# Optimization experiments

Hardware: AMD Instinct MI355X
Metric: run time of the kernel (lower is better)

Reference implementation:

```python
import jax, jax.numpy as jnp
import numpy as np

B, N, DIN = 32, 4096, 256
K, D, H = 8, 256, 512
ITERS = 3
EPS = 1e-8
LN_EPS = 1e-5
SCALE = D ** -0.5


def _ln(x, g, b):
    m = jnp.mean(x, axis=-1, keepdims=True)
    v = jnp.var(x, axis=-1, keepdims=True)
    return (x - m) * jax.lax.rsqrt(v + LN_EPS) * g + b


def setup_inputs() -> dict:
    key = jax.random.key(0)
    ks = jax.random.split(key, 12)
    lin = lambda k, o, i: jax.random.uniform(k, (o, i), jnp.float32, -1.0, 1.0) * (i ** -0.5)
    return {
        "x": jax.random.normal(ks[0], (B, N, DIN), jnp.float32),
        "noise": jax.random.normal(ks[1], (B, K, D), jnp.float32),
        "nx_g": jnp.ones((DIN,), jnp.float32), "nx_b": jnp.zeros((DIN,), jnp.float32),
        "ns_g": jnp.ones((D,), jnp.float32), "ns_b": jnp.zeros((D,), jnp.float32),
        "mu": jax.random.normal(ks[2], (1, 1, D), jnp.float32) * 0.02,
        "logsigma": jnp.zeros((1, 1, D), jnp.float32),
        "Wq": lin(ks[3], D, D), "Wk": lin(ks[4], D, DIN), "Wv": lin(ks[5], D, DIN),
        "W_ih": lin(ks[6], 3 * D, D), "W_hh": lin(ks[7], 3 * D, D),
        "b_ih": jnp.zeros((3 * D,), jnp.float32), "b_hh": jnp.zeros((3 * D,), jnp.float32),
        "mlp_g": jnp.ones((D,), jnp.float32), "mlp_b": jnp.zeros((D,), jnp.float32),
        "W1": lin(ks[8], H, D), "b1": jnp.zeros((H,), jnp.float32),
        "W2": lin(ks[9], D, H), "b2": jnp.zeros((D,), jnp.float32),
    }


def _gru(u, h, W_ih, W_hh, b_ih, b_hh):
    # PyTorch GRUCell: gates ordered (r, z, n)
    gi = u @ W_ih.T + b_ih   # [BK, 3D]
    gh = h @ W_hh.T + b_hh
    ir, iz, inn = jnp.split(gi, 3, axis=-1)
    hr, hz, hn = jnp.split(gh, 3, axis=-1)
    r = jax.nn.sigmoid(ir + hr)
    z = jax.nn.sigmoid(iz + hz)
    n = jnp.tanh(inn + r * hn)
    return (1.0 - z) * n + z * h


def reference(x, noise, nx_g, nx_b, ns_g, ns_b, mu, logsigma, Wq, Wk, Wv,
              W_ih, W_hh, b_ih, b_hh, mlp_g, mlp_b, W1, b1, W2, b2):
    xn = _ln(x, nx_g, nx_b)                       # [B,N,DIN]
    k = xn @ Wk.T                                 # [B,N,D]
    v = xn @ Wv.T                                 # [B,N,D]
    slots = mu + jnp.exp(logsigma) * noise        # [B,K,D]
    attn = None
    for _ in range(ITERS):
        s = _ln(slots, ns_g, ns_b)
        q = s @ Wq.T                              # [B,K,D]
        logits = jnp.einsum('bkd,bnd->bkn', q, k) * SCALE
        attn = jax.nn.softmax(logits, axis=1) + EPS   # softmax over slots
        attn = attn / jnp.sum(attn, axis=1, keepdims=True)
        updates = jnp.einsum('bkn,bnd->bkd', attn, v)
        h = _gru(updates.reshape(B * K, D), slots.reshape(B * K, D),
                 W_ih, W_hh, b_ih, b_hh).reshape(B, K, D)
        m = _ln(h, mlp_g, mlp_b)
        m = jax.nn.gelu(m @ W1.T + b1, approximate=False) @ W2.T + b2
        slots = h + m
    return slots, attn
```

## Files before the change

### kernel.cpp

```cpp
#include <hip/hip_runtime.h>
#include <hip/hip_bf16.h>
#include <math.h>

#define LN_EPS 1e-5f
#define EPSA 1e-8f
#define SCALE 0.0625f

typedef __attribute__((ext_vector_type(8))) short short8;
typedef __attribute__((ext_vector_type(4))) float f32x4;

__device__ inline void bf2x(unsigned int u, float& a, float& b) {
    union { unsigned int i; float f; } lo, hi;
    lo.i = u << 16; hi.i = u & 0xffff0000u;
    a = lo.f; b = hi.f;
}
__device__ inline float sigmoidf_(float x) { return 1.0f / (1.0f + expf(-x)); }
__device__ inline unsigned short f2bf(float f) {
    union { float f; unsigned int u; } v; v.f = f;
    unsigned int r = v.u + 0x7fffu + ((v.u >> 16) & 1u);
    return (unsigned short)(r >> 16);
}

__global__ __launch_bounds__(256) void row_stats(const float* __restrict__ x,
                                                 float* __restrict__ stats) {
    int w = threadIdx.x >> 6;
    int lane = threadIdx.x & 63;
    int r = blockIdx.x * 4 + w;
    const float4 xv = ((const float4*)(x + (size_t)r * 256))[lane];
    float s = xv.x + xv.y + xv.z + xv.w;
    float s2 = xv.x*xv.x + xv.y*xv.y + xv.z*xv.z + xv.w*xv.w;
    for (int off = 32; off > 0; off >>= 1) {
        s  += __shfl_down(s, off);
        s2 += __shfl_down(s2, off);
    }
    if (lane == 0) {
        float m = s * (1.0f/256.0f);
        float v = s2 * (1.0f/256.0f) - m * m;
        stats[2*r]   = m;
        stats[2*r+1] = rsqrtf(v + LN_EPS);
    }
}

__global__ __launch_bounds__(256) void pack_wb(const float* __restrict__ Wk,
                                               const float* __restrict__ Wv,
                                               __hip_bfloat16* __restrict__ Wcb) {
    int idx = blockIdx.x * 256 + threadIdx.x;
    int n = idx >> 8, k = idx & 255;
    float v = (n < 256) ? Wk[n*256 + k] : Wv[(n-256)*256 + k];
    Wcb[idx] = __float2bfloat16(v);
}

__global__ __launch_bounds__(256) void gemm_kv_mfma(const float* __restrict__ x,
                                                    const float* __restrict__ stats,
                                                    const float* __restrict__ nx_g,
                                                    const float* __restrict__ nx_b,
                                                    const __hip_bfloat16* __restrict__ Wcb,
                                                    __hip_bfloat16* __restrict__ kp,
                                                    __hip_bfloat16* __restrict__ vp) {
    __shared__ short As[128*64];
    __shared__ short Bs[128*64];
    const int t = threadIdx.x;
    const int row0 = blockIdx.x * 128;
    const int by = blockIdx.y;
    const int col0 = by * 128;
    const int l = t & 63, wid = t >> 6;
    const int wm = wid >> 1, wn = wid & 1;
    const int lr = l & 15, lk = (l >> 4) * 8;

    f32x4 acc[4][4];
    #pragma unroll
    for (int m = 0; m < 4; ++m)
        #pragma unroll
        for (int n = 0; n < 4; ++n) acc[m][n] = (f32x4){0.f, 0.f, 0.f, 0.f};

    for (int kt = 0; kt < 256; kt += 64) {
        #pragma unroll
        for (int j = 0; j < 4; ++j) {
            int g = j*256 + t;
            const __hip_bfloat16* src = Wcb + (size_t)(col0 + (g >> 3))*256 + kt + (g & 7)*8;
            __builtin_amdgcn_global_load_lds((const __attribute__((address_space(1))) void*)src,
                (__attribute__((address_space(3))) void*)(Bs + g*8), 16, 0, 0);
        }
        #pragma unroll
        for (int j = 0; j < 4; ++j) {
            int g = j*256 + t;
            int r = row0 + (g >> 3);
            int c = kt + (g & 7)*8;
            const float4* xs = (const float4*)(x + (size_t)r*256 + c);
            float4 v0 = xs[0], v1 = xs[1];
            float  mm = stats[2*r], rs = stats[2*r+1];
            const float4* gp = (const float4*)(nx_g + c);
            const float4* bp = (const float4*)(nx_b + c);
            float4 g0 = gp[0], g1 = gp[1], b0 = bp[0], b1 = bp[1];
            short8 o;
            o[0] = (short)f2bf((v0.x - mm)*rs*g0.x + b0.x);
            o[1] = (short)f2bf((v0.y - mm)*rs*g0.y + b0.y);
            o[2] = (short)f2bf((v0.z - mm)*rs*g0.z + b0.z);
            o[3] = (short)f2bf((v0.w - mm)*rs*g0.w + b0.w);
            o[4] = (short)f2bf((v1.x - mm)*rs*g1.x + b1.x);
            o[5] = (short)f2bf((v1.y - mm)*rs*g1.y + b1.y);
            o[6] = (short)f2bf((v1.z - mm)*rs*g1.z + b1.z);
            o[7] = (short)f2bf((v1.w - mm)*rs*g1.w + b1.w);
            *(short8*)&As[g*8] = o;
        }
        __syncthreads();

        #pragma unroll
        for (int kk = 0; kk < 64; kk += 32) {
            short8 af[4], bf[4];
            #pragma unroll
            for (int m = 0; m < 4; ++m)
                af[m] = *(const short8*)&As[(wm*64 + m*16 + lr)*64 + kk + lk];
            #pragma unroll
            for (int n = 0; n < 4; ++n)
                bf[n] = *(const short8*)&Bs[(wn*64 + n*16 + lr)*64 + kk + lk];
            #pragma unroll
            for (int m = 0; m < 4; ++m)
                #pragma unroll
                for (int n = 0; n < 4; ++n)
                    acc[m][n] = __builtin_amdgcn_mfma_f32_16x16x32_bf16(af[m], bf[n], acc[m][n], 0, 0, 0);
        }
        __syncthreads();
    }

    __hip_bfloat16* dst = (by < 2) ? kp : vp;
    const int colloc = col0 - ((by >= 2) ? 256 : 0);
    #pragma unroll
    for (int m = 0; m < 4; ++m)
        #pragma unroll
        for (int n = 0; n < 4; ++n) {
            #pragma unroll
            for (int jj = 0; jj < 4; ++jj) {
                int r = row0 + wm*64 + m*16 + (l >> 4)*4 + jj;
                int cc = colloc + wn*64 + n*16 + (l & 15);
                dst[(size_t)r*256 + cc] = __float2bfloat16(acc[m][n][jj]);
            }
        }
}

__global__ __launch_bounds__(256) void slots_init(const float* __restrict__ noise,
                                                  const float* __restrict__ mu,
                                                  const float* __restrict__ logsigma,
                                                  float* __restrict__ slots) {
    int i = blockIdx.x * 256 + threadIdx.x;
    int d = i & 255;
    slots[i] = mu[d] + expf(logsigma[d]) * noise[i];
}

__global__ __launch_bounds__(256) void qproj(const float* __restrict__ slots,
                                             const float* __restrict__ ns_g,
                                             const float* __restrict__ ns_b,
                                             const float* __restrict__ Wq,
                                             float* __restrict__ q) {
    int row = blockIdx.x, t = threadIdx.x;
    __shared__ float sn[256];
    __shared__ float red[8];
    float v = slots[row*256 + t];
    float s = v, s2 = v*v;
    for (int off = 32; off > 0; off >>= 1) {
        s  += __shfl_down(s, off);
        s2 += __shfl_down(s2, off);
    }
    if ((t & 63) == 0) { red[t>>6] = s; red[4 + (t>>6)] = s2; }
    __syncthreads();
    float S  = red[0]+red[1]+red[2]+red[3];
    float S2 = red[4]+red[5]+red[6]+red[7];
    float m = S * (1.0f/256.0f);
    float var = S2 * (1.0f/256.0f) - m*m;
    float rs = rsqrtf(var + LN_EPS);
    sn[t] = (v - m) * rs * ns_g[t] + ns_b[t];
    __syncthreads();
    float acc = 0.0f;
    const float4* wrow = (const float4*)(Wq + t*256);
    #pragma unroll 8
    for (int i = 0; i < 64; ++i) {
        float4 w = wrow[i];
        acc += w.x*sn[4*i] + w.y*sn[4*i+1] + w.z*sn[4*i+2] + w.w*sn[4*i+3];
    }
    q[row*256 + t] = acc;
}

__global__ __launch_bounds__(256) void attn_updates(const __hip_bfloat16* __restrict__ kp,
                                                    const __hip_bfloat16* __restrict__ vp,
                                                    const float* __restrict__ q,
                                                    float* __restrict__ attn_out,
                                                    float* __restrict__ partial) {
    int b = blockIdx.x >> 4, ch = blockIdx.x & 15, t = threadIdx.x;
    __shared__ float qs[8][256];
    __shared__ float as[8][256];
    #pragma unroll
    for (int j = 0; j < 8; ++j) qs[j][t] = q[(b*8 + j)*256 + t];
    __syncthreads();

    int n = ch*256 + t;
    const uint4* k4 = (const uint4*)(kp + ((size_t)b*4096 + n)*256);
    float lg[8] = {0,0,0,0,0,0,0,0};
    for (int i = 0; i < 32; ++i) {
        uint4 u = k4[i];
        float f[8];
        bf2x(u.x, f[0], f[1]); bf2x(u.y, f[2], f[3]);
        bf2x(u.z, f[4], f[5]); bf2x(u.w, f[6], f[7]);
        int d0 = i*8;
        #pragma unroll
        for (int kk = 0; kk < 8; ++kk) {
            float a = 0.0f;
            #pragma unroll
            for (int j = 0; j < 8; ++j) a += f[j] * qs[kk][d0 + j];
            lg[kk] += a;
        }
    }
    float mx = -1e30f;
    #pragma unroll
    for (int kk = 0; kk < 8; ++kk) { lg[kk] *= SCALE; mx = fmaxf(mx, lg[kk]); }
    float sum = 0.0f;
    #pragma unroll
    for (int kk = 0; kk < 8; ++kk) { lg[kk] = expf(lg[kk] - mx); sum += lg[kk]; }
    float inv = 1.0f / sum;
    const float renorm = 1.0f / (1.0f + 8.0f*EPSA);
    #pragma unroll
    for (int kk = 0; kk < 8; ++kk) {
        float a = (lg[kk]*inv + EPSA) * renorm;
        as[kk][t] = a;
        attn_out[((size_t)(b*8 + kk))*4096 + n] = a;
    }
    __syncthreads();

    int kk = t >> 5, dg = t & 31;
    float acc[8] = {0,0,0,0,0,0,0,0};
    const uint4* v4 = (const uint4*)(vp + ((size_t)b*4096 + ch*256)*256);
    #pragma unroll 4
    for (int nn = 0; nn < 256; ++nn) {
        float a = as[kk][nn];
        uint4 u = v4[nn*32 + dg];
        float f[8];
        bf2x(u.x, f[0], f[1]); bf2x(u.y, f[2], f[3]);
        bf2x(u.z, f[4], f[5]); bf2x(u.w, f[6], f[7]);
        #pragma unroll
        for (int j = 0; j < 8; ++j) acc[j] += a * f[j];
    }
    float* p = partial + (((size_t)(b*16 + ch)*8 + kk)*256) + dg*8;
    #pragma unroll
    for (int j = 0; j < 8; ++j) p[j] = acc[j];
}

__global__ __launch_bounds__(256) void gru(const float* __restrict__ partial,
                                           const float* __restrict__ slots,
                                           const float* __restrict__ W_ih,
                                           const float* __restrict__ W_hh,
                                           const float* __restrict__ b_ih,
                                           const float* __restrict__ b_hh,
                                           float* __restrict__ hprime) {
    int r = blockIdx.x, t = threadIdx.x;
    int b = r >> 3, k = r & 7;
    __shared__ float u_s[256], h_s[256];
    float u = 0.0f;
    #pragma unroll
    for (int ch = 0; ch < 16; ++ch)
        u += partial[(((size_t)(b*16 + ch)*8 + k)*256) + t];
    u_s[t] = u;
    h_s[t] = slots[r*256 + t];
    __syncthreads();

    float gi_r = b_ih[t], gi_z = b_ih[256 + t], gi_n = b_ih[512 + t];
    float gh_r = b_hh[t], gh_z = b_hh[256 + t], gh_n = b_hh[512 + t];
    const float4* wir = (const float4*)(W_ih + (size_t)t*256);
    const float4* wiz = (const float4*)(W_ih + (size_t)(256 + t)*256);
    const float4* win = (const float4*)(W_ih + (size_t)(512 + t)*256);
    const float4* whr = (const float4*)(W_hh + (size_t)t*256);
    const float4* whz = (const float4*)(W_hh + (size_t)(256 + t)*256);
    const float4* whn = (const float4*)(W_hh + (size_t)(512 + t)*256);
    #pragma unroll 4
    for (int i = 0; i < 64; ++i) {
        float u0 = u_s[4*i], u1 = u_s[4*i+1], u2 = u_s[4*i+2], u3 = u_s[4*i+3];
        float h0 = h_s[4*i], h1 = h_s[4*i+1], h2 = h_s[4*i+2], h3 = h_s[4*i+3];
        float4 w;
        w = wir[i]; gi_r += w.x*u0 + w.y*u1 + w.z*u2 + w.w*u3;
        w = wiz[i]; gi_z += w.x*u0 + w.y*u1 + w.z*u2 + w.w*u3;
        w = win[i]; gi_n += w.x*u0 + w.y*u1 + w.z*u2 + w.w*u3;
        w = whr[i]; gh_r += w.x*h0 + w.y*h1 + w.z*h2 + w.w*h3;
        w = whz[i]; gh_z += w.x*h0 + w.y*h1 + w.z*h2 + w.w*h3;
        w = whn[i]; gh_n += w.x*h0 + w.y*h1 + w.z*h2 + w.w*h3;
    }
    float rg = sigmoidf_(gi_r + gh_r);
    float zg = sigmoidf_(gi_z + gh_z);
    float ng = tanhf(gi_n + rg * gh_n);
    hprime[r*256 + t] = (1.0f - zg)*ng + zg*h_s[t];
}

__global__ __launch_bounds__(256) void mlp(const float* __restrict__ hprime,
                                           const float* __restrict__ mlp_g,
                                           const float* __restrict__ mlp_b,
                                           const float* __restrict__ W1,
                                           const float* __restrict__ b1,
                                           const float* __restrict__ W2,
                                           const float* __restrict__ b2,
                                           float* __restrict__ slots,
                                           float* __restrict__ out_slots,
                                           int last) {
    int r = blockIdx.x, t = threadIdx.x;
    __shared__ float hn[256];
    __shared__ float m1[512];
    __shared__ float red[8];
    float h = hprime[r*256 + t];
    float s = h, s2 = h*h;
    for (int off = 32; off > 0; off >>= 1) {
        s  += __shfl_down(s, off);
        s2 += __shfl_down(s2, off);
    }
    if ((t & 63) == 0) { red[t>>6] = s; red[4 + (t>>6)] = s2; }
    __syncthreads();
    float S  = red[0]+red[1]+red[2]+red[3];
    float S2 = red[4]+red[5]+red[6]+red[7];
    float m = S * (1.0f/256.0f);
    float var = S2 * (1.0f/256.0f) - m*m;
    float rs = rsqrtf(var + LN_EPS);
    hn[t] = (h - m) * rs * mlp_g[t] + mlp_b[t];
    __syncthreads();

    #pragma unroll
    for (int jj = 0; jj < 2; ++jj) {
        int j = t + jj*256;
        float acc = b1[j];
        const float4* w = (const float4*)(W1 + (size_t)j*256);
        #pragma unroll 8
        for (int i = 0; i < 64; ++i) {
            float4 wv = w[i];
            acc += wv.x*hn[4*i] + wv.y*hn[4*i+1] + wv.z*hn[4*i+2] + wv.w*hn[4*i+3];
        }
        m1[j] = 0.5f * acc * (1.0f + erff(acc * 0.70710678118654752f));
    }
    __syncthreads();

    float acc = b2[t];
    const float4* w2 = (const float4*)(W2 + (size_t)t*512);
    #pragma unroll 8
    for (int i = 0; i < 128; ++i) {
        float4 wv = w2[i];
        acc += wv.x*m1[4*i] + wv.y*m1[4*i+1] + wv.z*m1[4*i+2] + wv.w*m1[4*i+3];
    }
    float res = h + acc;
    slots[r*256 + t] = res;
    if (last) out_slots[r*256 + t] = res;
}

extern "C" void kernel_launch(void* const* d_in, const int* in_sizes, int n_in,
                              void* d_out, int out_size, void* d_ws, size_t ws_size,
                              hipStream_t stream) {
    const float* x        = (const float*)d_in[0];
    const float* noise    = (const float*)d_in[1];
    const float* nx_g     = (const float*)d_in[2];
    const float* nx_b     = (const float*)d_in[3];
    const float* ns_g     = (const float*)d_in[4];
    const float* ns_b     = (const float*)d_in[5];
    const float* mu       = (const float*)d_in[6];
    const float* logsigma = (const float*)d_in[7];
    const float* Wq       = (const float*)d_in[8];
    const float* Wk       = (const float*)d_in[9];
    const float* Wv       = (const float*)d_in[10];
    const float* W_ih     = (const float*)d_in[11];
    const float* W_hh     = (const float*)d_in[12];
    const float* b_ih     = (const float*)d_in[13];
    const float* b_hh     = (const float*)d_in[14];
    const float* mlp_g    = (const float*)d_in[15];
    const float* mlp_b    = (const float*)d_in[16];
    const float* W1       = (const float*)d_in[17];
    const float* b1       = (const float*)d_in[18];
    const float* W2       = (const float*)d_in[19];
    const float* b2       = (const float*)d_in[20];

    float* out_slots = (float*)d_out;
    float* out_attn  = (float*)d_out + 65536;

    char* ws = (char*)d_ws;
    float* stats = (float*)ws;
    __hip_bfloat16* Wcb = (__hip_bfloat16*)(stats + 262144);
    __hip_bfloat16* kp  = Wcb + 131072;
    __hip_bfloat16* vp  = kp + (size_t)33554432;
    float* slots  = (float*)(vp + (size_t)33554432);
    float* qbuf   = slots + 65536;
    float* partial= qbuf + 65536;
    float* hprime = partial + 1048576;

    row_stats<<<32768, 256, 0, stream>>>(x, stats);
    pack_wb<<<512, 256, 0, stream>>>(Wk, Wv, Wcb);
    dim3 g2(1024, 4);
    gemm_kv_mfma<<<g2, 256, 0, stream>>>(x, stats, nx_g, nx_b, Wcb, kp, vp);
    slots_init<<<256, 256, 0, stream>>>(noise, mu, logsigma, slots);

    for (int it = 0; it < 3; ++it) {
        qproj<<<256, 256, 0, stream>>>(slots, ns_g, ns_b, Wq, qbuf);
        attn_updates<<<512, 256, 0, stream>>>(kp, vp, qbuf, out_attn, partial);
        gru<<<256, 256, 0, stream>>>(partial, slots, W_ih, W_hh, b_ih, b_hh, hprime);
        mlp<<<256, 256, 0, stream>>>(hprime, mlp_g, mlp_b, W1, b1, W2, b2,
                                     slots, out_slots, it == 2);
    }
}
```

Measured before the change: 811.5 us.

## Fuse LayerNorm into KV GEMM, MFMA attention, and merge GRU with MLP

Removes the separate row-statistics pass by computing LayerNorm stats inside the K/V projection kernel, which now holds a full 64-row A tile in swizzled LDS and streams weights from global memory. Attention logits and the attention-weighted V sum move to bf16 MFMA, with q and attn split into high/low bf16 parts to preserve precision. The GRU and MLP kernels are merged to drop one launch and the hprime round trip. The risks are that V is loaded as a strided element gather and B operands bypass LDS.

Measured after the change: 836.1 us. +3.0%, slower.

```diff
diff --git a/kernel.cpp b/kernel.cpp
--- a/kernel.cpp
+++ b/kernel.cpp
@@ -7,39 +7,19 @@
 #define SCALE 0.0625f
 
 typedef __attribute__((ext_vector_type(8))) short short8;
+typedef __attribute__((ext_vector_type(4))) short short4_t;
 typedef __attribute__((ext_vector_type(4))) float f32x4;
 
-__device__ inline void bf2x(unsigned int u, float& a, float& b) {
-    union { unsigned int i; float f; } lo, hi;
-    lo.i = u << 16; hi.i = u & 0xffff0000u;
-    a = lo.f; b = hi.f;
-}
-__device__ inline float sigmoidf_(float x) { return 1.0f / (1.0f + expf(-x)); }
 __device__ inline unsigned short f2bf(float f) {
     union { float f; unsigned int u; } v; v.f = f;
     unsigned int r = v.u + 0x7fffu + ((v.u >> 16) & 1u);
     return (unsigned short)(r >> 16);
 }
-
-__global__ __launch_bounds__(256) void row_stats(const float* __restrict__ x,
-                                                 float* __restrict__ stats) {
-    int w = threadIdx.x >> 6;
-    int lane = threadIdx.x & 63;
-    int r = blockIdx.x * 4 + w;
-    const float4 xv = ((const float4*)(x + (size_t)r * 256))[lane];
-    float s = xv.x + xv.y + xv.z + xv.w;
-    float s2 = xv.x*xv.x + xv.y*xv.y + xv.z*xv.z + xv.w*xv.w;
-    for (int off = 32; off > 0; off >>= 1) {
-        s  += __shfl_down(s, off);
-        s2 += __shfl_down(s2, off);
-    }
-    if (lane == 0) {
-        float m = s * (1.0f/256.0f);
-        float v = s2 * (1.0f/256.0f) - m * m;
-        stats[2*r]   = m;
-        stats[2*r+1] = rsqrtf(v + LN_EPS);
-    }
-}
+__device__ inline float bf2f(unsigned short h) {
+    union { unsigned int u; float f; } v; v.u = ((unsigned int)h) << 16;
+    return v.f;
+}
+__device__ inline float sigmoidf_(float x) { return 1.0f / (1.0f + expf(-x)); }
 
 __global__ __launch_bounds__(256) void pack_wb(const float* __restrict__ Wk,
                                                const float* __restrict__ Wv,
@@ -50,92 +30,86 @@
     Wcb[idx] = __float2bfloat16(v);
 }
 
-__global__ __launch_bounds__(256) void gemm_kv_mfma(const float* __restrict__ x,
-                                                    const float* __restrict__ stats,
-                                                    const float* __restrict__ nx_g,
-                                                    const float* __restrict__ nx_b,
-                                                    const __hip_bfloat16* __restrict__ Wcb,
-                                                    __hip_bfloat16* __restrict__ kp,
-                                                    __hip_bfloat16* __restrict__ vp) {
-    __shared__ short As[128*64];
-    __shared__ short Bs[128*64];
+__global__ __launch_bounds__(256) void gemm_kv_fused(const float* __restrict__ x,
+                                                     const float* __restrict__ nx_g,
+                                                     const float* __restrict__ nx_b,
+                                                     const __hip_bfloat16* __restrict__ Wcb,
+                                                     __hip_bfloat16* __restrict__ kp,
+                                                     __hip_bfloat16* __restrict__ vp) {
+    __shared__ short As[64*256];
+    __shared__ float gb[512];
     const int t = threadIdx.x;
-    const int row0 = blockIdx.x * 128;
-    const int by = blockIdx.y;
-    const int col0 = by * 128;
-    const int l = t & 63, wid = t >> 6;
-    const int wm = wid >> 1, wn = wid & 1;
-    const int lr = l & 15, lk = (l >> 4) * 8;
-
-    f32x4 acc[4][4];
-    #pragma unroll
-    for (int m = 0; m < 4; ++m)
-        #pragma unroll
-        for (int n = 0; n < 4; ++n) acc[m][n] = (f32x4){0.f, 0.f, 0.f, 0.f};
-
-    for (int kt = 0; kt < 256; kt += 64) {
-        #pragma unroll
-        for (int j = 0; j < 4; ++j) {
-            int g = j*256 + t;
-            const __hip_bfloat16* src = Wcb + (size_t)(col0 + (g >> 3))*256 + kt + (g & 7)*8;
-            __builtin_amdgcn_global_load_lds((const __attribute__((address_space(1))) void*)src,
-                (__attribute__((address_space(3))) void*)(Bs + g*8), 16, 0, 0);
-        }
-        #pragma unroll
-        for (int j = 0; j < 4; ++j) {
-            int g = j*256 + t;
-            int r = row0 + (g >> 3);
-            int c = kt + (g & 7)*8;
-            const float4* xs = (const float4*)(x + (size_t)r*256 + c);
-            float4 v0 = xs[0], v1 = xs[1];
-            float  mm = stats[2*r], rs = stats[2*r+1];
-            const float4* gp = (const float4*)(nx_g + c);
-            const float4* bp = (const float4*)(nx_b + c);
-            float4 g0 = gp[0], g1 = gp[1], b0 = bp[0], b1 = bp[1];
-            short8 o;
-            o[0] = (short)f2bf((v0.x - mm)*rs*g0.x + b0.x);
-            o[1] = (short)f2bf((v0.y - mm)*rs*g0.y + b0.y);
-            o[2] = (short)f2bf((v0.z - mm)*rs*g0.z + b0.z);
-            o[3] = (short)f2bf((v0.w - mm)*rs*g0.w + b0.w);
-            o[4] = (short)f2bf((v1.x - mm)*rs*g1.x + b1.x);
-            o[5] = (short)f2bf((v1.y - mm)*rs*g1.y + b1.y);
-            o[6] = (short)f2bf((v1.z - mm)*rs*g1.z + b1.z);
-            o[7] = (short)f2bf((v1.w - mm)*rs*g1.w + b1.w);
-            *(short8*)&As[g*8] = o;
-        }
-        __syncthreads();
-
-        #pragma unroll
-        for (int kk = 0; kk < 64; kk += 32) {
-            short8 af[4], bf[4];
+    const int row0 = blockIdx.x * 64;
+    const int r = t >> 2, q = t & 3;
+
+    float4 xr[16];
+    const float* xrow = x + (size_t)(row0 + r) * 256 + q*4;
+    #pragma unroll
+    for (int j = 0; j < 16; ++j) xr[j] = *(const float4*)(xrow + j*16);
+    gb[t] = nx_g[t]; gb[t+256] = nx_b[t];
+
+    float s = 0.f, s2 = 0.f;
+    #pragma unroll
+    for (int j = 0; j < 16; ++j) {
+        s  += xr[j].x + xr[j].y + xr[j].z + xr[j].w;
+        s2 += xr[j].x*xr[j].x + xr[j].y*xr[j].y + xr[j].z*xr[j].z + xr[j].w*xr[j].w;
+    }
+    s  += __shfl_xor(s, 1);  s2 += __shfl_xor(s2, 1);
+    s  += __shfl_xor(s, 2);  s2 += __shfl_xor(s2, 2);
+    float m = s * (1.0f/256.0f);
+    float var = s2 * (1.0f/256.0f) - m*m;
+    float rstd = rsqrtf(var + LN_EPS);
+    __syncthreads();
+
+    #pragma unroll
+    for (int j = 0; j < 16; ++j) {
+        int c = q*4 + j*16;
+        float4 g = *(const float4*)&gb[c];
+        float4 bb = *(const float4*)&gb[256 + c];
+        short4_t o;
+        o[0] = (short)f2bf((xr[j].x - m)*rstd*g.x + bb.x);
+        o[1] = (short)f2bf((xr[j].y - m)*rstd*g.y + bb.y);
+        o[2] = (short)f2bf((xr[j].z - m)*rstd*g.z + bb.z);
+        o[3] = (short)f2bf((xr[j].w - m)*rstd*g.w + bb.w);
+        int byte = ((r << 9) + (c << 1)) ^ ((r & 7) << 4);
+        *(short4_t*)((char*)As + byte) = o;
+    }
+    __syncthreads();
+
+    const int l = t & 63, w = t >> 6;
+    const int lr = l & 15, lk = l >> 4;
+    const int arow = w*16 + lr;
+    short8 af[8];
+    #pragma unroll
+    for (int ks = 0; ks < 8; ++ks) {
+        int lin = (arow << 9) + (lk << 4) + (ks << 6);
+        af[ks] = *(short8*)((char*)As + (lin ^ ((arow & 7) << 4)));
+    }
+    for (int c = 0; c < 8; ++c) {
+        f32x4 acc[4];
+        #pragma unroll
+        for (int bf = 0; bf < 4; ++bf) acc[bf] = (f32x4){0.f,0.f,0.f,0.f};
+        #pragma unroll
+        for (int ks = 0; ks < 8; ++ks) {
             #pragma unroll
-            for (int m = 0; m < 4; ++m)
-                af[m] = *(const short8*)&As[(wm*64 + m*16 + lr)*64 + kk + lk];
-            #pragma unroll
-            for (int n = 0; n < 4; ++n)
-                bf[n] = *(const short8*)&Bs[(wn*64 + n*16 + lr)*64 + kk + lk];
-            #pragma unroll
-            for (int m = 0; m < 4; ++m)
-                #pragma unroll
-                for (int n = 0; n < 4; ++n)
-                    acc[m][n] = __builtin_amdgcn_mfma_f32_16x16x32_bf16(af[m], bf[n], acc[m][n], 0, 0, 0);
-        }
-        __syncthreads();
-    }
-
-    __hip_bfloat16* dst = (by < 2) ? kp : vp;
-    const int colloc = col0 - ((by >= 2) ? 256 : 0);
-    #pragma unroll
-    for (int m = 0; m < 4; ++m)
-        #pragma unroll
-        for (int n = 0; n < 4; ++n) {
+            for (int bf = 0; bf < 4; ++bf) {
+                const short8 bv = *(const short8*)((const short*)Wcb +
+                    ((size_t)(c*64 + bf*16 + lr))*256 + ks*32 + lk*8);
+                acc[bf] = __builtin_amdgcn_mfma_f32_16x16x32_bf16(af[ks], bv, acc[bf], 0, 0, 0);
+            }
+        }
+        __hip_bfloat16* dst = (c < 4) ? kp : vp;
+        const int cb = c*64 - ((c >= 4) ? 256 : 0);
+        #pragma unroll
+        for (int bf = 0; bf < 4; ++bf) {
+            int col = cb + bf*16 + lr;
             #pragma unroll
             for (int jj = 0; jj < 4; ++jj) {
-                int r = row0 + wm*64 + m*16 + (l >> 4)*4 + jj;
-                int cc = colloc + wn*64 + n*16 + (l & 15);
-                dst[(size_t)r*256 + cc] = __float2bfloat16(acc[m][n][jj]);
+                int row = row0 + w*16 + lk*4 + jj;
+                dst[(size_t)row*256 + col] = __float2bfloat16(acc[bf][jj]);
             }
         }
+    }
 }
 
 __global__ __launch_bounds__(256) void slots_init(const float* __restrict__ noise,
@@ -151,8 +125,9 @@
                                              const float* __restrict__ ns_g,
                                              const float* __restrict__ ns_b,
                                              const float* __restrict__ Wq,
-                                             float* __restrict__ q) {
+                                             unsigned short* __restrict__ qb) {
     int row = blockIdx.x, t = threadIdx.x;
+    int b = row >> 3, s8 = row & 7;
     __shared__ float sn[256];
     __shared__ float red[8];
     float v = slots[row*256 + t];
@@ -177,88 +152,147 @@
         float4 w = wrow[i];
         acc += w.x*sn[4*i] + w.y*sn[4*i+1] + w.z*sn[4*i+2] + w.w*sn[4*i+3];
     }
-    q[row*256 + t] = acc;
-}
-
-__global__ __launch_bounds__(256) void attn_updates(const __hip_bfloat16* __restrict__ kp,
-                                                    const __hip_bfloat16* __restrict__ vp,
-                                                    const float* __restrict__ q,
-                                                    float* __restrict__ attn_out,
-                                                    float* __restrict__ partial) {
-    int b = blockIdx.x >> 4, ch = blockIdx.x & 15, t = threadIdx.x;
-    __shared__ float qs[8][256];
-    __shared__ float as[8][256];
-    #pragma unroll
-    for (int j = 0; j < 8; ++j) qs[j][t] = q[(b*8 + j)*256 + t];
-    __syncthreads();
-
-    int n = ch*256 + t;
-    const uint4* k4 = (const uint4*)(kp + ((size_t)b*4096 + n)*256);
-    float lg[8] = {0,0,0,0,0,0,0,0};
-    for (int i = 0; i < 32; ++i) {
-        uint4 u = k4[i];
-        float f[8];
-        bf2x(u.x, f[0], f[1]); bf2x(u.y, f[2], f[3]);
-        bf2x(u.z, f[4], f[5]); bf2x(u.w, f[6], f[7]);
-        int d0 = i*8;
-        #pragma unroll
-        for (int kk = 0; kk < 8; ++kk) {
-            float a = 0.0f;
+    unsigned short hh = f2bf(acc);
+    unsigned short ll = f2bf(acc - bf2f(hh));
+    qb[((size_t)(b*16 + s8))*256 + t]     = hh;
+    qb[((size_t)(b*16 + 8 + s8))*256 + t] = ll;
+}
+
+__global__ __launch_bounds__(256) void attn_fused(const __hip_bfloat16* __restrict__ kp,
+                                                  const __hip_bfloat16* __restrict__ vp,
+                                                  const unsigned short* __restrict__ qb,
+                                                  float* __restrict__ attn_out,
+                                                  float* __restrict__ partial) {
+    __shared__ short as_[16*264];
+    __shared__ float asf[8*256];
+    const int b = blockIdx.x >> 4, c = blockIdx.x & 15;
+    const int t = threadIdx.x, l = t & 63, w = t >> 6;
+    const int lr = l & 15, lk = l >> 4;
+    const int n0 = c * 256;
+
+    short8 qf[8];
+    #pragma unroll
+    for (int ks = 0; ks < 8; ++ks)
+        qf[ks] = *(const short8*)(qb + ((size_t)(b*16 + lr))*256 + ks*32 + lk*8);
+
+    f32x4 acc[4];
+    #pragma unroll
+    for (int nf = 0; nf < 4; ++nf) acc[nf] = (f32x4){0.f,0.f,0.f,0.f};
+    #pragma unroll
+    for (int ks = 0; ks < 8; ++ks) {
+        #pragma unroll
+        for (int nf = 0; nf < 4; ++nf) {
+            const short8 a = *(const short8*)((const short*)kp +
+                ((size_t)(b*4096 + n0 + w*64 + nf*16 + lr))*256 + ks*32 + lk*8);
+            acc[nf] = __builtin_amdgcn_mfma_f32_16x16x32_bf16(a, qf[ks], acc[nf], 0, 0, 0);
+        }
+    }
+
+    const float renorm = 1.0f / (1.0f + 8.0f*EPSA);
+    #pragma unroll
+    for (int nf = 0; nf < 4; ++nf) {
+        #pragma unroll
+        for (int jj = 0; jj < 4; ++jj) {
+            float lg = acc[nf][jj];
+            lg += __shfl_xor(lg, 8);
+            lg *= SCALE;
+            float mx = lg;
+            mx = fmaxf(mx, __shfl_xor(mx, 1));
+            mx = fmaxf(mx, __shfl_xor(mx, 2));
+            mx = fmaxf(mx, __shfl_xor(mx, 4));
+            float e = expf(lg - mx);
+            float ss = e;
+            ss += __shfl_xor(ss, 1);
+            ss += __shfl_xor(ss, 2);
+            ss += __shfl_xor(ss, 4);
+            acc[nf][jj] = (e / ss + EPSA) * renorm;
+        }
+    }
+
+    if (lr < 8) {
+        #pragma unroll
+        for (int nf = 0; nf < 4; ++nf) {
+            int nl = w*64 + nf*16 + lk*4;
+            float4 fa = {acc[nf][0], acc[nf][1], acc[nf][2], acc[nf][3]};
+            *(float4*)&asf[lr*256 + nl] = fa;
+            short4_t ah, al;
             #pragma unroll
-            for (int j = 0; j < 8; ++j) a += f[j] * qs[kk][d0 + j];
-            lg[kk] += a;
-        }
-    }
-    float mx = -1e30f;
-    #pragma unroll
-    for (int kk = 0; kk < 8; ++kk) { lg[kk] *= SCALE; mx = fmaxf(mx, lg[kk]); }
-    float sum = 0.0f;
-    #pragma unroll
-    for (int kk = 0; kk < 8; ++kk) { lg[kk] = expf(lg[kk] - mx); sum += lg[kk]; }
-    float inv = 1.0f / sum;
-    const float renorm = 1.0f / (1.0f + 8.0f*EPSA);
-    #pragma unroll
-    for (int kk = 0; kk < 8; ++kk) {
-        float a = (lg[kk]*inv + EPSA) * renorm;
-        as[kk][t] = a;
-        attn_out[((size_t)(b*8 + kk))*4096 + n] = a;
-    }
-    __syncthreads();
-
-    int kk = t >> 5, dg = t & 31;
-    float acc[8] = {0,0,0,0,0,0,0,0};
-    const uint4* v4 = (const uint4*)(vp + ((size_t)b*4096 + ch*256)*256);
-    #pragma unroll 4
-    for (int nn = 0; nn < 256; ++nn) {
-        float a = as[kk][nn];
-        uint4 u = v4[nn*32 + dg];
-        float f[8];
-        bf2x(u.x, f[0], f[1]); bf2x(u.y, f[2], f[3]);
-        bf2x(u.z, f[4], f[5]); bf2x(u.w, f[6], f[7]);
-        #pragma unroll
-        for (int j = 0; j < 8; ++j) acc[j] += a * f[j];
-    }
-    float* p = partial + (((size_t)(b*16 + ch)*8 + kk)*256) + dg*8;
-    #pragma unroll
-    for (int j = 0; j < 8; ++j) p[j] = acc[j];
-}
-
-__global__ __launch_bounds__(256) void gru(const float* __restrict__ partial,
-                                           const float* __restrict__ slots,
-                                           const float* __restrict__ W_ih,
-                                           const float* __restrict__ W_hh,
-                                           const float* __restrict__ b_ih,
-                                           const float* __restrict__ b_hh,
-                                           float* __restrict__ hprime) {
-    int r = blockIdx.x, t = threadIdx.x;
-    int b = r >> 3, k = r & 7;
+            for (int jj = 0; jj < 4; ++jj) {
+                unsigned short h = f2bf(acc[nf][jj]);
+                ah[jj] = (short)h;
+                al[jj] = (short)f2bf(acc[nf][jj] - bf2f(h));
+            }
+            *(short4_t*)&as_[lr*264 + nl]       = ah;
+            *(short4_t*)&as_[(8 + lr)*264 + nl] = al;
+        }
+    }
+    __syncthreads();
+
+    {
+        int slot = t >> 5, nn = (t & 31) * 8;
+        float4 f0 = *(float4*)&asf[slot*256 + nn];
+        float4 f1 = *(float4*)&asf[slot*256 + nn + 4];
+        float* dstp = attn_out + ((size_t)(b*8 + slot))*4096 + n0 + nn;
+        *(float4*)dstp = f0;
+        *(float4*)(dstp + 4) = f1;
+    }
+
+    f32x4 pacc[4];
+    #pragma unroll
+    for (int df = 0; df < 4; ++df) pacc[df] = (f32x4){0.f,0.f,0.f,0.f};
+    #pragma unroll
+    for (int ks = 0; ks < 8; ++ks) {
+        const short8 a = *(const short8*)&as_[lr*264 + ks*32 + lk*8];
+        #pragma unroll
+        for (int df = 0; df < 4; ++df) {
+            short8 bv;
+            #pragma unroll
+            for (int j = 0; j < 8; ++j)
+                bv[j] = ((const short*)vp)[((size_t)(b*4096 + n0 + ks*32 + lk*8 + j))*256
+                                           + w*64 + df*16 + lr];
+            pacc[df] = __builtin_amdgcn_mfma_f32_16x16x32_bf16(a, bv, pacc[df], 0, 0, 0);
+        }
+    }
+    #pragma unroll
+    for (int df = 0; df < 4; ++df) {
+        #pragma unroll
+        for (int jj = 0; jj < 4; ++jj) {
+            float v = pacc[df][jj];
+            float vo = __shfl_xor(v, 32);
+            if (l < 32) {
+                int slot = lk*4 + jj;
+                partial[((size_t)((b*16 + c)*8 + slot))*256 + w*64 + df*16 + lr] = v + vo;
+            }
+        }
+    }
+}
+
+__global__ __launch_bounds__(256) void gru_mlp(const float* __restrict__ partial,
+                                               const float* __restrict__ slots,
+                                               const float* __restrict__ W_ih,
+                                               const float* __restrict__ W_hh,
+                                               const float* __restrict__ b_ih,
+                                               const float* __restrict__ b_hh,
+                                               const float* __restrict__ mlp_g,
+                                               const float* __restrict__ mlp_b,
+                                               const float* __restrict__ W1,
+                                               const float* __restrict__ b1,
+                                               const float* __restrict__ W2,
+                                               const float* __restrict__ b2,
+                                               float* __restrict__ slots_out,
+                                               float* __restrict__ out_slots,
+                                               int last) {
+    int rrow = blockIdx.x, t = threadIdx.x;
+    int b = rrow >> 3, k = rrow & 7;
     __shared__ float u_s[256], h_s[256];
+    __shared__ float hn[256], m1[512];
+    __shared__ float red[8];
     float u = 0.0f;
     #pragma unroll
     for (int ch = 0; ch < 16; ++ch)
         u += partial[(((size_t)(b*16 + ch)*8 + k)*256) + t];
     u_s[t] = u;
-    h_s[t] = slots[r*256 + t];
+    h_s[t] = slots[rrow*256 + t];
     __syncthreads();
 
     float gi_r = b_ih[t], gi_z = b_ih[256 + t], gi_n = b_ih[512 + t];
@@ -273,40 +307,25 @@
     for (int i = 0; i < 64; ++i) {
         float u0 = u_s[4*i], u1 = u_s[4*i+1], u2 = u_s[4*i+2], u3 = u_s[4*i+3];
         float h0 = h_s[4*i], h1 = h_s[4*i+1], h2 = h_s[4*i+2], h3 = h_s[4*i+3];
-        float4 w;
-        w = wir[i]; gi_r += w.x*u0 + w.y*u1 + w.z*u2 + w.w*u3;
-        w = wiz[i]; gi_z += w.x*u0 + w.y*u1 + w.z*u2 + w.w*u3;
-        w = win[i]; gi_n += w.x*u0 + w.y*u1 + w.z*u2 + w.w*u3;
-        w = whr[i]; gh_r += w.x*h0 + w.y*h1 + w.z*h2 + w.w*h3;
-        w = whz[i]; gh_z += w.x*h0 + w.y*h1 + w.z*h2 + w.w*h3;
-        w = whn[i]; gh_n += w.x*h0 + w.y*h1 + w.z*h2 + w.w*h3;
+        float4 wv;
+        wv = wir[i]; gi_r += wv.x*u0 + wv.y*u1 + wv.z*u2 + wv.w*u3;
+        wv = wiz[i]; gi_z += wv.x*u0 + wv.y*u1 + wv.z*u2 + wv.w*u3;
+        wv = win[i]; gi_n += wv.x*u0 + wv.y*u1 + wv.z*u2 + wv.w*u3;
+        wv = whr[i]; gh_r += wv.x*h0 + wv.y*h1 + wv.z*h2 + wv.w*h3;
+        wv = whz[i]; gh_z += wv.x*h0 + wv.y*h1 + wv.z*h2 + wv.w*h3;
+        wv = whn[i]; gh_n += wv.x*h0 + wv.y*h1 + wv.z*h2 + wv.w*h3;
     }
     float rg = sigmoidf_(gi_r + gh_r);
     float zg = sigmoidf_(gi_z + gh_z);
     float ng = tanhf(gi_n + rg * gh_n);
-    hprime[r*256 + t] = (1.0f - zg)*ng + zg*h_s[t];
-}
-
-__global__ __launch_bounds__(256) void mlp(const float* __restrict__ hprime,
-                                           const float* __restrict__ mlp_g,
-                                           const float* __restrict__ mlp_b,
-                                           const float* __restrict__ W1,
-                                           const float* __restrict__ b1,
-                                           const float* __restrict__ W2,
-                                           const float* __restrict__ b2,
-                                           float* __restrict__ slots,
-                                           float* __restrict__ out_slots,
-                                           int last) {
-    int r = blockIdx.x, t = threadIdx.x;
-    __shared__ float hn[256];
-    __shared__ float m1[512];
-    __shared__ float red[8];
-    float h = hprime[r*256 + t];
-    float s = h, s2 = h*h;
+    float hval = (1.0f - zg)*ng + zg*h_s[t];
+
+    float s = hval, s2 = hval*hval;
     for (int off = 32; off > 0; off >>= 1) {
         s  += __shfl_down(s, off);
         s2 += __shfl_down(s2, off);
     }
+    __syncthreads();
     if ((t & 63) == 0) { red[t>>6] = s; red[4 + (t>>6)] = s2; }
     __syncthreads();
     float S  = red[0]+red[1]+red[2]+red[3];
@@ -314,18 +333,18 @@
     float m = S * (1.0f/256.0f);
     float var = S2 * (1.0f/256.0f) - m*m;
     float rs = rsqrtf(var + LN_EPS);
-    hn[t] = (h - m) * rs * mlp_g[t] + mlp_b[t];
+    hn[t] = (hval - m) * rs * mlp_g[t] + mlp_b[t];
     __syncthreads();
 
     #pragma unroll
     for (int jj = 0; jj < 2; ++jj) {
         int j = t + jj*256;
         float acc = b1[j];
-        const float4* w = (const float4*)(W1 + (size_t)j*256);
+        const float4* wv = (const float4*)(W1 + (size_t)j*256);
         #pragma unroll 8
         for (int i = 0; i < 64; ++i) {
-            float4 wv = w[i];
-            acc += wv.x*hn[4*i] + wv.y*hn[4*i+1] + wv.z*hn[4*i+2] + wv.w*hn[4*i+3];
+            float4 ww = wv[i];
+            acc += ww.x*hn[4*i] + ww.y*hn[4*i+1] + ww.z*hn[4*i+2] + ww.w*hn[4*i+3];
         }
         m1[j] = 0.5f * acc * (1.0f + erff(acc * 0.70710678118654752f));
     }
@@ -335,12 +354,12 @@
     const float4* w2 = (const float4*)(W2 + (size_t)t*512);
     #pragma unroll 8
     for (int i = 0; i < 128; ++i) {
-        float4 wv = w2[i];
-        acc += wv.x*m1[4*i] + wv.y*m1[4*i+1] + wv.z*m1[4*i+2] + wv.w*m1[4*i+3];
-    }
-    float res = h + acc;
-    slots[r*256 + t] = res;
-    if (last) out_slots[r*256 + t] = res;
+        float4 ww = w2[i];
+        acc += ww.x*m1[4*i] + ww.y*m1[4*i+1] + ww.z*m1[4*i+2] + ww.w*m1[4*i+3];
+    }
+    float res = hval + acc;
+    slots_out[rrow*256 + t] = res;
+    if (last) out_slots[rrow*256 + t] = res;
 }
 
 extern "C" void kernel_launch(void* const* d_in, const int* in_sizes, int n_in,
@@ -372,26 +391,22 @@
     float* out_attn  = (float*)d_out + 65536;
 
     char* ws = (char*)d_ws;
-    float* stats = (float*)ws;
-    __hip_bfloat16* Wcb = (__hip_bfloat16*)(stats + 262144);
-    __hip_bfloat16* kp  = Wcb + 131072;
+    __hip_bfloat16* Wcb = (__hip_bfloat16*)ws;
+    unsigned short* qb  = (unsigned short*)(Wcb + 131072);
+    __hip_bfloat16* kp  = (__hip_bfloat16*)(qb + 131072);
     __hip_bfloat16* vp  = kp + (size_t)33554432;
     float* slots  = (float*)(vp + (size_t)33554432);
-    float* qbuf   = slots + 65536;
-    float* partial= qbuf + 65536;
-    float* hprime = partial + 1048576;
-
-    row_stats<<<32768, 256, 0, stream>>>(x, stats);
+    float* partial= slots + 65536;
+
     pack_wb<<<512, 256, 0, stream>>>(Wk, Wv, Wcb);
-    dim3 g2(1024, 4);
-    gemm_kv_mfma<<<g2, 256, 0, stream>>>(x, stats, nx_g, nx_b, Wcb, kp, vp);
+    gemm_kv_fused<<<2048, 256, 0, stream>>>(x, nx_g, nx_b, Wcb, kp, vp);
     slots_init<<<256, 256, 0, stream>>>(noise, mu, logsigma, slots);
 
     for (int it = 0; it < 3; ++it) {
-        qproj<<<256, 256, 0, stream>>>(slots, ns_g, ns_b, Wq, qbuf);
-        attn_updates<<<512, 256, 0, stream>>>(kp, vp, qbuf, out_attn, partial);
-        gru<<<256, 256, 0, stream>>>(partial, slots, W_ih, W_hh, b_ih, b_hh, hprime);
-        mlp<<<256, 256, 0, stream>>>(hprime, mlp_g, mlp_b, W1, b1, W2, b2,
-                                     slots, out_slots, it == 2);
-    }
-}
+        qproj<<<256, 256, 0, stream>>>(slots, ns_g, ns_b, Wq, qb);
+        attn_fused<<<512, 256, 0, stream>>>(kp, vp, qb, out_attn, partial);
+        gru_mlp<<<256, 256, 0, stream>>>(partial, slots, W_ih, W_hh, b_ih, b_hh,
+                                         mlp_g, mlp_b, W1, b1, W2, b2,
+                                         slots, out_slots, it == 2);
+    }
+}
```
